# Performance work log

Measured on AMD Instinct MI355X. Metric: run time of the kernel, lower is better.

## Reference

```python
import jax, jax.numpy as jnp
import numpy as np

B, C, D, H, W = 2, 8, 64, 160, 160


def setup_inputs() -> dict:
    key = jax.random.key(0)
    k1, k2, k3 = jax.random.split(key, 3)
    net_output = jax.random.normal(k1, (B, C, D, H, W), dtype=jnp.float32)
    # sample 0 only contains classes {0..4} (partial labels), sample 1 all 8 classes,
    # so the dynamic task-merging / channel-padding paths are exercised.
    lab0 = jax.random.randint(k2, (1, D, H, W), 0, 5)
    lab1 = jax.random.randint(k3, (1, D, H, W), 0, C)
    labels = jnp.concatenate([lab0, lab1], axis=0)  # [B,D,H,W]
    target = jax.nn.one_hot(labels, C, dtype=jnp.float32).transpose(0, 4, 1, 2, 3)
    return {"net_output": net_output, "target": target}


def reference(net_output, target):
    # Masked (non-compacted) re-expression of DC_CE_Marginal_loss.
    # Original pipeline: partial_onehot compacts target to the per-sample
    # present classes (sorted, background first) and zero-pads to the batch
    # max L; merge_prediction adds logits of absent classes into background;
    # softmax_fun softmaxes each sample over its valid channels only; dice is
    # averaged over valid channels; CE uses full softmax over L channels where
    # the (L - n_i) padding channels carry logit 0 and target 0.  All of this
    # is channel-permutation invariant, so we compute it in the original
    # channel layout with a presence mask and account for the zero-logit
    # padding channels analytically.
    Cc = net_output.shape[1]
    labels = jnp.argmax(target, axis=1)  # [B,D,H,W]
    counts = jax.vmap(lambda l: jnp.bincount(l.ravel(), length=Cc))(labels)  # [B,C]
    present = counts > 0
    pm = present.astype(net_output.dtype)[:, :, None, None, None]  # [B,C,1,1,1]

    # merge_prediction: absent foreground logits folded into background
    bg_extra = jnp.sum(net_output[:, 1:] * (1.0 - pm[:, 1:]), axis=1, keepdims=True)
    m = jnp.concatenate([net_output[:, :1] + bg_extra, net_output[:, 1:]], axis=1)
    t_eff = target * pm  # compacted target (absent channels dropped)

    n = jnp.sum(present, axis=1).astype(net_output.dtype)  # valid channels / sample
    pad = jnp.max(n) - n  # number of zero-logit padding channels / sample

    zm = jnp.where(pm > 0, m, -jnp.inf)  # logits restricted to present classes
    # ---- cross entropy over L = max(n) channels (padding logits are 0) ----
    lse_p = jax.nn.logsumexp(zm, axis=1)  # [B,D,H,W]
    lse = jnp.where((pad > 0)[:, None, None, None],
                    jnp.logaddexp(lse_p, jnp.log(jnp.maximum(pad, 1.0))[:, None, None, None]),
                    lse_p)
    ce_loss = jnp.mean(lse - jnp.sum(t_eff * m, axis=1))

    # ---- dice over per-sample valid channels (softmax over present only) ----
    p = jax.nn.softmax(zm, axis=1)  # absent channels -> 0 (softmax_fun)
    ref_vol = jnp.sum(t_eff, axis=(2, 3, 4))      # [B,C]
    seg_vol = jnp.sum(p, axis=(2, 3, 4))
    intersect = jnp.sum(t_eff * p, axis=(2, 3, 4))
    dice_c = 2.0 * intersect / (ref_vol + seg_vol + 1e-5)
    dice_i = 1.0 - jnp.sum(present * dice_c, axis=1) / n  # mean over valid channels
    dc_loss = jnp.mean(dice_i)

    return 0.5 * ce_loss + 0.5 * dc_loss
```

## Files before the change

### kernel.cpp

```cpp
#include <hip/hip_runtime.h>
#include <math.h>

#define BB 2
#define CC 8
#define DD 64
#define HH 160
#define WW 160
#define SS (DD*HH*WW)
#define NVOX (BB*SS)
#define THREADS 256
#define GPT 4
#define BLOCKS_PER_SAMPLE (SS/(THREADS*4*GPT))
#define NBLOCKS (BB*BLOCKS_PER_SAMPLE)

#define L2E 1.4426950408889634f
#define LN2 0.6931471805599453f

typedef float f32x4 __attribute__((ext_vector_type(4)));

__global__ __launch_bounds__(THREADS)
void pass_label(const f32x4* __restrict__ tgt,
                unsigned short* __restrict__ lab16,
                unsigned int* __restrict__ cnt_part) {
    __shared__ unsigned int scnt[CC];
    const int tid = threadIdx.x;
    if (tid < CC) scnt[tid] = 0u;
    __syncthreads();

    const int b   = blockIdx.x / BLOCKS_PER_SAMPLE;
    const int blk = blockIdx.x % BLOCKS_PER_SAMPLE;
    const int S4  = SS / 4;
    const f32x4* base = tgt + (size_t)b * CC * S4;
    unsigned short* lab = lab16 + (size_t)b * S4;

    for (int it = 0; it < GPT; ++it) {
        const int g = blk * (THREADS * GPT) + it * THREADS + tid;
        f32x4 v[CC];
        #pragma unroll
        for (int c = 0; c < CC; ++c) v[c] = __builtin_nontemporal_load(base + (size_t)c * S4 + g);

        int l0 = 0, l1 = 0, l2 = 0, l3 = 0;
        #pragma unroll
        for (int c = 1; c < CC; ++c) {
            if (v[c][0] > 0.5f) l0 = c;
            if (v[c][1] > 0.5f) l1 = c;
            if (v[c][2] > 0.5f) l2 = c;
            if (v[c][3] > 0.5f) l3 = c;
        }
        lab[g] = (unsigned short)(l0 | (l1 << 4) | (l2 << 8) | (l3 << 12));
        atomicAdd(&scnt[l0], 1u);
        atomicAdd(&scnt[l1], 1u);
        atomicAdd(&scnt[l2], 1u);
        atomicAdd(&scnt[l3], 1u);
    }
    __syncthreads();
    if (tid < CC) cnt_part[tid * NBLOCKS + blockIdx.x] = scnt[tid];
}

__global__ __launch_bounds__(THREADS)
void pass_main(const f32x4* __restrict__ net,
               const unsigned short* __restrict__ lab16,
               const unsigned int* __restrict__ cnt_part,
               float* __restrict__ part) {
    __shared__ unsigned int sc[2 * CC];
    __shared__ float s_red[2 * CC + 1];

    const int tid = threadIdx.x;
    const int b   = blockIdx.x / BLOCKS_PER_SAMPLE;
    const int blk = blockIdx.x % BLOCKS_PER_SAMPLE;

    {
        const int w = tid >> 6, lane = tid & 63;
        const int c   = 2 * w + (lane >> 5);
        const int sub = lane & 31;
        const unsigned int* col = cnt_part + c * NBLOCKS;
        unsigned int a0 = 0, a1 = 0;
        #pragma unroll
        for (int i = 0; i < NBLOCKS / 32; ++i) {
            const int idx = sub + (i << 5);
            const unsigned int v = col[idx];
            if (idx < BLOCKS_PER_SAMPLE) a0 += v; else a1 += v;
        }
        #pragma unroll
        for (int off = 16; off > 0; off >>= 1) {
            a0 += __shfl_down(a0, off, 64);
            a1 += __shfl_down(a1, off, 64);
        }
        if (sub == 0) { sc[c] = a0; sc[CC + c] = a1; }
    }
    if (tid < 2 * CC + 1) s_red[tid] = 0.0f;
    __syncthreads();

    int n0 = 0, n1 = 0;
    #pragma unroll
    for (int c = 0; c < CC; ++c) { n0 += (sc[c] > 0u); n1 += (sc[CC + c] > 0u); }
    const int maxn = n0 > n1 ? n0 : n1;
    const float padf = (float)(maxn - ((b == 0) ? n0 : n1));
    float ab[CC], bias[CC];
    #pragma unroll
    for (int c = 0; c < CC; ++c) {
        ab[c]   = (sc[b * CC + c] > 0u) ? 0.0f : 1.0f;
        bias[c] = -2048.0f * ab[c];
    }

    float segA[CC];
    float intA[CC];
    #pragma unroll
    for (int c = 0; c < CC; ++c) { segA[c] = 0.0f; intA[c] = 0.0f; }
    float ceA = 0.0f;

    const int S4 = SS / 4;
    const f32x4* base = net + (size_t)b * CC * S4;
    const unsigned short* lab = lab16 + (size_t)b * S4;

    for (int it = 0; it < GPT; ++it) {
        const int g = blk * (THREADS * GPT) + it * THREADS + tid;
        f32x4 v[CC];
        #pragma unroll
        for (int c = 0; c < CC; ++c) v[c] = __builtin_nontemporal_load(base + (size_t)c * S4 + g);
        const unsigned int Lp = lab[g];

        #pragma unroll
        for (int j = 0; j < 4; ++j) {
            const int lab_j = (Lp >> (4 * j)) & 0xF;
            float m[CC];
            m[0] = v[0][j];
            float f1 = ab[1] * v[1][j];
            float f2 = ab[2] * v[2][j];
            float f3 = ab[3] * v[3][j];
            float f4 = ab[4] * v[4][j];
            float f5 = ab[5] * v[5][j];
            float f6 = ab[6] * v[6][j];
            float f7 = ab[7] * v[7][j];
            #pragma unroll
            for (int c = 1; c < CC; ++c) m[c] = v[c][j];
            m[0] += ((f1 + f2) + (f3 + f4)) + ((f5 + f6) + f7);

            float e[CC];
            #pragma unroll
            for (int c = 0; c < CC; ++c)
                e[c] = __builtin_amdgcn_exp2f(fmaf(m[c], L2E, bias[c]));
            const float sp = ((e[0] + e[1]) + (e[2] + e[3])) + ((e[4] + e[5]) + (e[6] + e[7]));
            const float se = sp + padf;
            const float lse = LN2 * __builtin_amdgcn_logf(se);

            float inv = __builtin_amdgcn_rcpf(sp);
            inv = inv * (2.0f - sp * inv);

            float mlab = 0.0f;
            #pragma unroll
            for (int c = 0; c < CC; ++c) {
                const float p = e[c] * inv;
                segA[c] += p;
                const bool isl = (lab_j == c);
                intA[c] += isl ? p : 0.0f;
                mlab     = isl ? m[c] : mlab;
            }
            ceA += lse - mlab;
        }
    }

    #pragma unroll
    for (int off = 32; off > 0; off >>= 1) {
        #pragma unroll
        for (int c = 0; c < CC; ++c) {
            segA[c] += __shfl_down(segA[c], off, 64);
            intA[c] += __shfl_down(intA[c], off, 64);
        }
        ceA += __shfl_down(ceA, off, 64);
    }
    if ((tid & 63) == 0) {
        #pragma unroll
        for (int c = 0; c < CC; ++c) {
            atomicAdd(&s_red[c],      segA[c]);
            atomicAdd(&s_red[CC + c], intA[c]);
        }
        atomicAdd(&s_red[2 * CC], ceA);
    }
    __syncthreads();
    if (tid < 2 * CC + 1) part[tid * NBLOCKS + blockIdx.x] = s_red[tid];
}

__global__ __launch_bounds__(512)
void finalize(const unsigned int* __restrict__ cnt_part,
              const float* __restrict__ part,
              float* __restrict__ out) {
    __shared__ float sred[2 * CC + 1][2];
    __shared__ unsigned int sc[2 * CC];
    const int tid = threadIdx.x;
    const int w = tid >> 6, lane = tid & 63;

    for (int q = w; q < 2 * CC + 1; q += 8) {
        float a0 = 0.0f, a1 = 0.0f;
        const float* col = part + q * NBLOCKS;
        #pragma unroll
        for (int k = 0; k < 13; ++k) {
            const int idx = lane + (k << 6);
            if (idx < NBLOCKS) {
                const float v = col[idx];
                if (idx < BLOCKS_PER_SAMPLE) a0 += v; else a1 += v;
            }
        }
        #pragma unroll
        for (int off = 32; off > 0; off >>= 1) {
            a0 += __shfl_down(a0, off, 64);
            a1 += __shfl_down(a1, off, 64);
        }
        if (lane == 0) { sred[q][0] = a0; sred[q][1] = a1; }
    }
    {
        unsigned int a0 = 0, a1 = 0;
        const unsigned int* col = cnt_part + w * NBLOCKS;
        #pragma unroll
        for (int k = 0; k < 13; ++k) {
            const int idx = lane + (k << 6);
            if (idx < NBLOCKS) {
                const unsigned int v = col[idx];
                if (idx < BLOCKS_PER_SAMPLE) a0 += v; else a1 += v;
            }
        }
        #pragma unroll
        for (int off = 32; off > 0; off >>= 1) {
            a0 += __shfl_down(a0, off, 64);
            a1 += __shfl_down(a1, off, 64);
        }
        if (lane == 0) { sc[w] = a0; sc[CC + w] = a1; }
    }
    __syncthreads();
    if (tid == 0) {
        const float ce = (sred[2 * CC][0] + sred[2 * CC][1]) / (float)NVOX;
        float dc = 0.0f;
        for (int b = 0; b < BB; ++b) {
            int nb = 0;
            float acc = 0.0f;
            for (int c = 0; c < CC; ++c) {
                const unsigned int cnt = sc[b * CC + c];
                if (cnt > 0u) {
                    ++nb;
                    const float R = (float)cnt;
                    const float Sg = sred[c][b];
                    const float I  = sred[CC + c][b];
                    acc += 2.0f * I / (R + Sg + 1e-5f);
                }
            }
            dc += 1.0f - acc / (float)nb;
        }
        dc /= (float)BB;
        out[0] = 0.5f * ce + 0.5f * dc;
    }
}

extern "C" void kernel_launch(void* const* d_in, const int* in_sizes, int n_in,
                              void* d_out, int out_size, void* d_ws, size_t ws_size,
                              hipStream_t stream) {
    const f32x4* net = (const f32x4*)d_in[0];
    const f32x4* tgt = (const f32x4*)d_in[1];
    float* out = (float*)d_out;

    unsigned int*   cnt_part = (unsigned int*)d_ws;
    float*          part     = (float*)((char*)d_ws + 25600);
    unsigned short* lab16    = (unsigned short*)((char*)d_ws + 80000);

    pass_label<<<NBLOCKS, THREADS, 0, stream>>>(tgt, lab16, cnt_part);
    pass_main<<<NBLOCKS, THREADS, 0, stream>>>(net, lab16, cnt_part, part);
    finalize<<<1, 512, 0, stream>>>(cnt_part, part, out);
}
```

Measured before the change: 48.42 us.

## Use per-block presence bitmasks and prefetch first tile before mask reduction

The label pass now writes a per-block bitmask of present classes, so the main pass reduces one OR-mask per block instead of summing eight count columns. The main pass issues its first group of logit loads before the presence reduction and its barrier, overlapping that memory latency with the setup. GPT is halved, which doubles the block count and gives more parallelism but also more per-block setup and a longer finalize reduction. Workspace offsets are reshuffled to fit the larger partial arrays.

```diff
diff --git a/kernel.cpp b/kernel.cpp
--- a/kernel.cpp
+++ b/kernel.cpp
@@ -9,7 +9,7 @@
 #define SS (DD*HH*WW)
 #define NVOX (BB*SS)
 #define THREADS 256
-#define GPT 4
+#define GPT 2
 #define BLOCKS_PER_SAMPLE (SS/(THREADS*4*GPT))
 #define NBLOCKS (BB*BLOCKS_PER_SAMPLE)
 
@@ -21,7 +21,8 @@
 __global__ __launch_bounds__(THREADS)
 void pass_label(const f32x4* __restrict__ tgt,
                 unsigned short* __restrict__ lab16,
-                unsigned int* __restrict__ cnt_part) {
+                unsigned int* __restrict__ cnt_part,
+                unsigned int* __restrict__ pb) {
     __shared__ unsigned int scnt[CC];
     const int tid = threadIdx.x;
     if (tid < CC) scnt[tid] = 0u;
@@ -55,70 +56,83 @@
     }
     __syncthreads();
     if (tid < CC) cnt_part[tid * NBLOCKS + blockIdx.x] = scnt[tid];
+    if (tid == 0) {
+        unsigned int mask = 0;
+        #pragma unroll
+        for (int c = 0; c < CC; ++c) mask |= (scnt[c] > 0u) ? (1u << c) : 0u;
+        pb[blockIdx.x] = mask;
+    }
 }
 
 __global__ __launch_bounds__(THREADS)
 void pass_main(const f32x4* __restrict__ net,
                const unsigned short* __restrict__ lab16,
-               const unsigned int* __restrict__ cnt_part,
+               const unsigned int* __restrict__ pb,
                float* __restrict__ part) {
-    __shared__ unsigned int sc[2 * CC];
+    __shared__ unsigned int smask[2];
     __shared__ float s_red[2 * CC + 1];
 
     const int tid = threadIdx.x;
     const int b   = blockIdx.x / BLOCKS_PER_SAMPLE;
     const int blk = blockIdx.x % BLOCKS_PER_SAMPLE;
 
-    {
-        const int w = tid >> 6, lane = tid & 63;
-        const int c   = 2 * w + (lane >> 5);
-        const int sub = lane & 31;
-        const unsigned int* col = cnt_part + c * NBLOCKS;
-        unsigned int a0 = 0, a1 = 0;
-        #pragma unroll
-        for (int i = 0; i < NBLOCKS / 32; ++i) {
-            const int idx = sub + (i << 5);
-            const unsigned int v = col[idx];
-            if (idx < BLOCKS_PER_SAMPLE) a0 += v; else a1 += v;
-        }
-        #pragma unroll
-        for (int off = 16; off > 0; off >>= 1) {
-            a0 += __shfl_down(a0, off, 64);
-            a1 += __shfl_down(a1, off, 64);
-        }
-        if (sub == 0) { sc[c] = a0; sc[CC + c] = a1; }
-    }
+    if (tid < 2) smask[tid] = 0u;
     if (tid < 2 * CC + 1) s_red[tid] = 0.0f;
     __syncthreads();
-
-    int n0 = 0, n1 = 0;
-    #pragma unroll
-    for (int c = 0; c < CC; ++c) { n0 += (sc[c] > 0u); n1 += (sc[CC + c] > 0u); }
-    const int maxn = n0 > n1 ? n0 : n1;
-    const float padf = (float)(maxn - ((b == 0) ? n0 : n1));
-    float ab[CC], bias[CC];
-    #pragma unroll
-    for (int c = 0; c < CC; ++c) {
-        ab[c]   = (sc[b * CC + c] > 0u) ? 0.0f : 1.0f;
-        bias[c] = -2048.0f * ab[c];
-    }
-
-    float segA[CC];
-    float intA[CC];
-    #pragma unroll
-    for (int c = 0; c < CC; ++c) { segA[c] = 0.0f; intA[c] = 0.0f; }
-    float ceA = 0.0f;
 
     const int S4 = SS / 4;
     const f32x4* base = net + (size_t)b * CC * S4;
     const unsigned short* lab = lab16 + (size_t)b * S4;
 
+    const int g0 = blk * (THREADS * GPT) + tid;
+    f32x4 v0[CC];
+    #pragma unroll
+    for (int c = 0; c < CC; ++c) v0[c] = __builtin_nontemporal_load(base + (size_t)c * S4 + g0);
+    const unsigned int Lp0 = lab[g0];
+
+    {
+        unsigned int om0 = 0, om1 = 0;
+        for (int i = tid; i < NBLOCKS; i += THREADS) {
+            const unsigned int m = pb[i];
+            if (i < BLOCKS_PER_SAMPLE) om0 |= m; else om1 |= m;
+        }
+        if (om0) atomicOr(&smask[0], om0);
+        if (om1) atomicOr(&smask[1], om1);
+    }
+    __syncthreads();
+
+    const unsigned int mask0 = smask[0], mask1 = smask[1];
+    const int n0 = __popc(mask0), n1 = __popc(mask1);
+    const int maxn = n0 > n1 ? n0 : n1;
+    const float padf = (float)(maxn - ((b == 0) ? n0 : n1));
+    const unsigned int maskb = (b == 0) ? mask0 : mask1;
+    float ab[CC], bias[CC];
+    #pragma unroll
+    for (int c = 0; c < CC; ++c) {
+        ab[c]   = ((maskb >> c) & 1u) ? 0.0f : 1.0f;
+        bias[c] = -2048.0f * ab[c];
+    }
+
+    float segA[CC];
+    float intA[CC];
+    #pragma unroll
+    for (int c = 0; c < CC; ++c) { segA[c] = 0.0f; intA[c] = 0.0f; }
+    float ceA = 0.0f;
+
+    #pragma unroll
     for (int it = 0; it < GPT; ++it) {
-        const int g = blk * (THREADS * GPT) + it * THREADS + tid;
         f32x4 v[CC];
-        #pragma unroll
-        for (int c = 0; c < CC; ++c) v[c] = __builtin_nontemporal_load(base + (size_t)c * S4 + g);
-        const unsigned int Lp = lab[g];
+        unsigned int Lp;
+        if (it == 0) {
+            #pragma unroll
+            for (int c = 0; c < CC; ++c) v[c] = v0[c];
+            Lp = Lp0;
+        } else {
+            const int g = blk * (THREADS * GPT) + it * THREADS + tid;
+            #pragma unroll
+            for (int c = 0; c < CC; ++c) v[c] = __builtin_nontemporal_load(base + (size_t)c * S4 + g);
+            Lp = lab[g];
+        }
 
         #pragma unroll
         for (int j = 0; j < 4; ++j) {
@@ -194,12 +208,10 @@
         float a0 = 0.0f, a1 = 0.0f;
         const float* col = part + q * NBLOCKS;
         #pragma unroll
-        for (int k = 0; k < 13; ++k) {
+        for (int k = 0; k < NBLOCKS / 64; ++k) {
             const int idx = lane + (k << 6);
-            if (idx < NBLOCKS) {
-                const float v = col[idx];
-                if (idx < BLOCKS_PER_SAMPLE) a0 += v; else a1 += v;
-            }
+            const float v = col[idx];
+            if (idx < BLOCKS_PER_SAMPLE) a0 += v; else a1 += v;
         }
         #pragma unroll
         for (int off = 32; off > 0; off >>= 1) {
@@ -212,12 +224,10 @@
         unsigned int a0 = 0, a1 = 0;
         const unsigned int* col = cnt_part + w * NBLOCKS;
         #pragma unroll
-        for (int k = 0; k < 13; ++k) {
+        for (int k = 0; k < NBLOCKS / 64; ++k) {
             const int idx = lane + (k << 6);
-            if (idx < NBLOCKS) {
-                const unsigned int v = col[idx];
-                if (idx < BLOCKS_PER_SAMPLE) a0 += v; else a1 += v;
-            }
+            const unsigned int v = col[idx];
+            if (idx < BLOCKS_PER_SAMPLE) a0 += v; else a1 += v;
         }
         #pragma unroll
         for (int off = 32; off > 0; off >>= 1) {
@@ -258,10 +268,11 @@
     float* out = (float*)d_out;
 
     unsigned int*   cnt_part = (unsigned int*)d_ws;
-    float*          part     = (float*)((char*)d_ws + 25600);
-    unsigned short* lab16    = (unsigned short*)((char*)d_ws + 80000);
-
-    pass_label<<<NBLOCKS, THREADS, 0, stream>>>(tgt, lab16, cnt_part);
-    pass_main<<<NBLOCKS, THREADS, 0, stream>>>(net, lab16, cnt_part, part);
+    unsigned int*   pb       = (unsigned int*)((char*)d_ws + 51200);
+    float*          part     = (float*)((char*)d_ws + 57600);
+    unsigned short* lab16    = (unsigned short*)((char*)d_ws + 166400);
+
+    pass_label<<<NBLOCKS, THREADS, 0, stream>>>(tgt, lab16, cnt_part, pb);
+    pass_main<<<NBLOCKS, THREADS, 0, stream>>>(net, lab16, pb, part);
     finalize<<<1, 512, 0, stream>>>(cnt_part, part, out);
 }
```

Measured after the change: 56.43 us. 16.5% more time.
